# Kernel optimization log

Measured on AMD Instinct MI355X. Metric: run time of the kernel, lower is better.

## Reference

```python
import jax, jax.numpy as jnp
import numpy as np

N, E, H, C = 50000, 800000, 4, 64   # nodes, edges, heads, per-head channels
EMB, VOCAB, G, RD, OUT = 128, 512, 64, 64, 1
LEAKY_SLOPE = 0.2


def _gat_layer(h_in, src, dst, W, att_src, att_dst, bias):
    """PyG GATConv, concat=False (mean over heads), eval mode (no dropout)."""
    n = h_in.shape[0]
    h = (h_in @ W).reshape(n, H, C)                       # [N,H,C]
    a_src = jnp.sum(h * att_src, axis=-1)                 # [N,H]
    a_dst = jnp.sum(h * att_dst, axis=-1)                 # [N,H]
    e = jax.nn.leaky_relu(a_src[src] + a_dst[dst], LEAKY_SLOPE)  # [E',H]
    # segment softmax over incoming edges of each destination node
    m = jax.ops.segment_max(e, dst, num_segments=n)       # [N,H]
    m = jnp.where(jnp.isfinite(m), m, 0.0)
    p = jnp.exp(e - m[dst])                               # [E',H]
    s = jax.ops.segment_sum(p, dst, num_segments=n)       # [N,H]
    alpha = p / (s[dst] + 1e-16)                          # [E',H]
    msg = alpha[:, :, None] * h[src]                      # [E',H,C]
    out = jax.ops.segment_sum(msg, dst, num_segments=n)   # [N,H,C]
    return out.mean(axis=1) + bias                        # [N,C]


def setup_inputs() -> dict:
    key = jax.random.key(0)
    ks = jax.random.split(key, 16)
    x = jax.random.randint(ks[0], (N, 2), 0, VOCAB)
    edge_index = jax.random.randint(ks[1], (2, E), 0, N)
    batch = jnp.sort(jax.random.randint(ks[2], (N,), 0, G))
    f32 = jnp.float32
    emb = jax.random.normal(ks[3], (VOCAB, EMB), f32) * (EMB ** -0.5)
    W0 = jax.random.normal(ks[4], (EMB, H * C), f32) * (EMB ** -0.5)
    as0 = jax.random.normal(ks[5], (H, C), f32) * (C ** -0.5)
    ad0 = jax.random.normal(ks[6], (H, C), f32) * (C ** -0.5)
    b0 = jnp.zeros((C,), f32)
    W1 = jax.random.normal(ks[7], (C, H * C), f32) * (C ** -0.5)
    as1 = jax.random.normal(ks[8], (H, C), f32) * (C ** -0.5)
    ad1 = jax.random.normal(ks[9], (H, C), f32) * (C ** -0.5)
    b1 = jnp.zeros((C,), f32)
    W2 = jax.random.normal(ks[10], (C, H * C), f32) * (C ** -0.5)
    as2 = jax.random.normal(ks[11], (H, C), f32) * (C ** -0.5)
    ad2 = jax.random.normal(ks[12], (H, C), f32) * (C ** -0.5)
    b2 = jnp.zeros((C,), f32)
    mW1 = jax.random.normal(ks[13], (C, C), f32) * (C ** -0.5)
    mb1 = jnp.zeros((C,), f32)
    mW2 = jax.random.normal(ks[14], (C, RD), f32) * (C ** -0.5)
    mb2 = jnp.zeros((RD,), f32)
    rW = jax.random.normal(ks[15], (RD, OUT), f32) * (RD ** -0.5)
    rb = jnp.zeros((OUT,), f32)
    return dict(x=x, edge_index=edge_index, batch=batch, emb=emb,
                W0=W0, as0=as0, ad0=ad0, b0=b0,
                W1=W1, as1=as1, ad1=ad1, b1=b1,
                W2=W2, as2=as2, ad2=ad2, b2=b2,
                mW1=mW1, mb1=mb1, mW2=mW2, mb2=mb2, rW=rW, rb=rb)


def reference(x, edge_index, batch, emb,
              W0, as0, ad0, b0,
              W1, as1, ad1, b1,
              W2, as2, ad2, b2,
              mW1, mb1, mW2, mb2, rW, rb):
    n = x.shape[0]
    # add self-loops (PyG GATConv default)
    loops = jnp.arange(n)
    src = jnp.concatenate([edge_index[0], loops])
    dst = jnp.concatenate([edge_index[1], loops])

    h = emb[x[:, 0]]                                      # [N,EMB]
    h = jax.nn.elu(_gat_layer(h, src, dst, W0, as0, ad0, b0))
    h = jax.nn.elu(_gat_layer(h, src, dst, W1, as1, ad1, b1))
    h = jax.nn.elu(_gat_layer(h, src, dst, W2, as2, ad2, b2))

    # global mean pool per graph
    sums = jax.ops.segment_sum(h, batch, num_segments=G)  # [G,C]
    cnt = jax.ops.segment_sum(jnp.ones((n,), h.dtype), batch, num_segments=G)
    pooled = sums / jnp.maximum(cnt, 1.0)[:, None]

    # MLP readout: Linear -> ELU -> Linear (plain last, eval: no dropout)
    r = jax.nn.elu(pooled @ mW1 + mb1)
    r = r @ mW2 + mb2
    return r @ rW + rb                                     # [G,OUT]
```

## Files before the change

kernel.cpp:

```cpp
#include <hip/hip_runtime.h>
#include <hip/hip_bf16.h>

#define TPB 256
#define CHUNK 8


__global__ void gather_emb_k(const int* __restrict__ x, const float* __restrict__ emb,
                             float* __restrict__ h0, int n) {
  int idx = blockIdx.x * TPB + threadIdx.x;
  if (idx >= n * 128) return;
  int node = idx >> 7, k = idx & 127;
  h0[idx] = emb[x[node * 2] * 128 + k];
}

__global__ void edge_hist_k(const int* __restrict__ ei, int* __restrict__ deg, int E, int n) {
  int e = blockIdx.x * TPB + threadIdx.x;
  if (e >= E + n) return;
  int dst = (e < E) ? ei[E + e] : (e - E);
  atomicAdd(&deg[dst], 1);
}

__global__ void scan_block_k(const int* __restrict__ deg, int* __restrict__ row_ptr,
                             int* __restrict__ bsum, int n) {
  __shared__ int buf[TPB];
  int t = threadIdx.x, base = blockIdx.x * TPB;
  int v = (base + t < n) ? deg[base + t] : 0;
  buf[t] = v;
  __syncthreads();
  for (int off = 1; off < TPB; off <<= 1) {
    int xv = (t >= off) ? buf[t - off] : 0;
    __syncthreads();
    buf[t] += xv;
    __syncthreads();
  }
  if (base + t < n) row_ptr[base + t + 1] = buf[t];
  if (t == TPB - 1) bsum[blockIdx.x] = buf[t];
}

__global__ void scan_bsum_k(int* __restrict__ bsum, int B) {
  __shared__ int buf[TPB];
  int t = threadIdx.x;
  int v = (t < B) ? bsum[t] : 0;
  buf[t] = v;
  __syncthreads();
  for (int off = 1; off < TPB; off <<= 1) {
    int xv = (t >= off) ? buf[t - off] : 0;
    __syncthreads();
    buf[t] += xv;
    __syncthreads();
  }
  if (t < B) bsum[t] = buf[t] - v;
}

__global__ void scan_add_k(int* __restrict__ row_ptr, const int* __restrict__ bsum, int n) {
  int idx = blockIdx.x * TPB + threadIdx.x;
  if (idx == 0) row_ptr[0] = 0;
  if (idx < n) row_ptr[idx + 1] += bsum[idx >> 8];
}

__global__ void edge_scatter_k(const int* __restrict__ ei, const int* __restrict__ row_ptr,
                               int* __restrict__ cursor, int* __restrict__ csr_src,
                               int E, int n) {
  int e = blockIdx.x * TPB + threadIdx.x;
  if (e >= E + n) return;
  int src, dst;
  if (e < E) { src = ei[e]; dst = ei[E + e]; }
  else       { src = e - E; dst = e - E; }
  int pos = atomicAdd(&cursor[dst], 1);
  csr_src[row_ptr[dst] + pos] = src;
}

template <int K>
__global__ __launch_bounds__(TPB) void gemm_hw_k(const float* __restrict__ h,
                                                 const float* __restrict__ W,
                                                 float* __restrict__ hW, int n) {
  int t = threadIdx.x;
  int n0 = blockIdx.x * 16;
  float acc[16];
#pragma unroll
  for (int i = 0; i < 16; i++) acc[i] = 0.f;
  const float* hb = h + (size_t)n0 * K;
  for (int k0 = 0; k0 < K; k0 += 8) {
    float wv[8];
#pragma unroll
    for (int kk = 0; kk < 8; kk++) wv[kk] = W[(k0 + kk) * 256 + t];
#pragma unroll
    for (int i = 0; i < 16; i++) {
#pragma unroll
      for (int kk = 0; kk < 8; kk++)
        acc[i] = fmaf(hb[i * K + k0 + kk], wv[kk], acc[i]);
    }
  }
  float* outp = hW + (size_t)n0 * 256 + t;
#pragma unroll
  for (int i = 0; i < 16; i++)
    if (n0 + i < n) outp[i * 256] = acc[i];
}

__global__ void attn_coef_k(const float* __restrict__ hW, const float* __restrict__ as,
                            const float* __restrict__ ad, float* __restrict__ a_srcv,
                            float* __restrict__ a_dstv, int n) {
  int idx = blockIdx.x * TPB + threadIdx.x;
  if (idx >= n * 4) return;
  int node = idx >> 2, hh = idx & 3;
  const float* row = hW + (size_t)node * 256 + hh * 64;
  const float* asr = as + hh * 64;
  const float* adr = ad + hh * 64;
  float s = 0.f, d = 0.f;
#pragma unroll 8
  for (int c = 0; c < 64; c++) {
    float v = row[c];
    s = fmaf(v, asr[c], s);
    d = fmaf(v, adr[c], d);
  }
  a_srcv[idx] = s;
  a_dstv[idx] = d;
}

__global__ __launch_bounds__(TPB) void gat_agg_k(
    const float* __restrict__ hW, const float* __restrict__ a_srcv,
    const float* __restrict__ a_dstv, const int* __restrict__ row_ptr,
    const int* __restrict__ csr_src, const float* __restrict__ bias,
    float* __restrict__ h_out, int n) {
  int node = blockIdx.x;
  int t = threadIdx.x;
  int w = t >> 6;
  int l = t & 63;
  int hh = l >> 4;
  int beg = row_ptr[node], end = row_ptr[node + 1];
  float ad = a_dstv[node * 4 + hh];

  float m = -1e30f, ssum = 0.f;
  float ax = 0.f, ay = 0.f, az = 0.f, aw = 0.f;

  for (int base = beg + w; base < end; base += 4 * CHUNK) {
    int   ss[CHUNK];
    float ee[CHUNK];
    float4 hv[CHUNK];
#pragma unroll
    for (int j = 0; j < CHUNK; j++) {
      int k = base + j * 4;
      ss[j] = (k < end) ? csr_src[k] : -1;
    }
#pragma unroll
    for (int j = 0; j < CHUNK; j++) {
      if (ss[j] >= 0) {
        float e = a_srcv[ss[j] * 4 + hh] + ad;
        ee[j] = (e >= 0.f) ? e : 0.2f * e;
        hv[j] = *reinterpret_cast<const float4*>(hW + (size_t)ss[j] * 256 + l * 4);
      } else {
        ee[j] = -1e30f;
        hv[j] = make_float4(0.f, 0.f, 0.f, 0.f);
      }
    }
#pragma unroll
    for (int j = 0; j < CHUNK; j++) {
      float e = ee[j];
      float diff = e - m;
      float ex = __expf(-fabsf(diff));
      bool nm = diff > 0.f;
      float scale = nm ? ex : 1.f;
      float p     = nm ? 1.f : ex;
      m = nm ? e : m;
      ssum = fmaf(ssum, scale, p);
      ax = fmaf(ax, scale, p * hv[j].x);
      ay = fmaf(ay, scale, p * hv[j].y);
      az = fmaf(az, scale, p * hv[j].z);
      aw = fmaf(aw, scale, p * hv[j].w);
    }
  }

  __shared__ float m_sh[4][4];
  __shared__ float s_sh[4][4];
  __shared__ float red[4][256];
  if ((l & 15) == 0) m_sh[w][hh] = m;
  __syncthreads();
  float mt = fmaxf(fmaxf(m_sh[0][hh], m_sh[1][hh]), fmaxf(m_sh[2][hh], m_sh[3][hh]));
  float sc = __expf(m - mt);
  if ((l & 15) == 0) s_sh[w][hh] = ssum * sc;
  float* rw = &red[w][l * 4];
  rw[0] = ax * sc; rw[1] = ay * sc; rw[2] = az * sc; rw[3] = aw * sc;
  __syncthreads();

  if (t < 64) {
    float o = 0.f;
#pragma unroll
    for (int h = 0; h < 4; ++h) {
      int cc = h * 64 + t;
      float v = red[0][cc] + red[1][cc] + red[2][cc] + red[3][cc];
      float st = s_sh[0][h] + s_sh[1][h] + s_sh[2][h] + s_sh[3][h];
      o += v / (st + 1e-16f);
    }
    o = o * 0.25f + bias[t];
    o = (o > 0.f) ? o : (expf(o) - 1.f);
    h_out[node * 64 + t] = o;
  }
}

__global__ void group_bounds_k(const int* __restrict__ batch, int* __restrict__ gstart,
                               int G_, int n) {
  int i = blockIdx.x * TPB + threadIdx.x;
  if (i >= n) return;
  if (i == 0) {
    int b0 = batch[0];
    for (int g = 0; g <= b0; ++g) gstart[g] = 0;
  } else {
    int bp = batch[i - 1], bc = batch[i];
    for (int g = bp + 1; g <= bc; ++g) gstart[g] = i;
  }
  if (i == n - 1) {
    int bl = batch[n - 1];
    for (int g = bl + 1; g <= G_; ++g) gstart[g] = n;
  }
}

__global__ void pool_group_k(const float* __restrict__ h, const int* __restrict__ gstart,
                             float* __restrict__ pooled) {
  int g = blockIdx.x, t = threadIdx.x;
  int c = t & 63, sub = t >> 6;
  int beg = gstart[g], end = gstart[g + 1];
  float s = 0.f;
  for (int i = beg + sub; i < end; i += 4) s += h[(size_t)i * 64 + c];
  __shared__ float red[4][64];
  red[sub][c] = s;
  __syncthreads();
  if (t < 64) {
    float v = red[0][t] + red[1][t] + red[2][t] + red[3][t];
    float cn = fmaxf((float)(end - beg), 1.f);
    pooled[g * 64 + t] = v / cn;
  }
}

__global__ void readout_k(const float* __restrict__ pooled,
                          const float* __restrict__ mW1, const float* __restrict__ mb1,
                          const float* __restrict__ mW2, const float* __restrict__ mb2,
                          const float* __restrict__ rW, const float* __restrict__ rb,
                          float* __restrict__ out) {
  int g = blockIdx.x, t = threadIdx.x;
  __shared__ float pm[64], r1[64], r2[64];
  pm[t] = pooled[g * 64 + t];
  __syncthreads();
  float a = mb1[t];
  for (int c = 0; c < 64; c++) a = fmaf(pm[c], mW1[c * 64 + t], a);
  a = (a > 0.f) ? a : (expf(a) - 1.f);
  r1[t] = a;
  __syncthreads();
  float b = mb2[t];
  for (int c = 0; c < 64; c++) b = fmaf(r1[c], mW2[c * 64 + t], b);
  r2[t] = b;
  __syncthreads();
  if (t == 0) {
    float o = rb[0];
    for (int c = 0; c < 64; c++) o = fmaf(r2[c], rW[c], o);
    out[g] = o;
  }
}

extern "C" void kernel_launch(void* const* d_in, const int* in_sizes, int n_in,
                              void* d_out, int out_size, void* d_ws, size_t ws_size,
                              hipStream_t stream) {
  const int* x     = (const int*)d_in[0];
  const int* ei    = (const int*)d_in[1];
  const int* batch = (const int*)d_in[2];
  const float* emb = (const float*)d_in[3];
  const float* W0  = (const float*)d_in[4];
  const float* as0 = (const float*)d_in[5];
  const float* ad0 = (const float*)d_in[6];
  const float* b0  = (const float*)d_in[7];
  const float* W1  = (const float*)d_in[8];
  const float* as1 = (const float*)d_in[9];
  const float* ad1 = (const float*)d_in[10];
  const float* b1  = (const float*)d_in[11];
  const float* W2  = (const float*)d_in[12];
  const float* as2 = (const float*)d_in[13];
  const float* ad2 = (const float*)d_in[14];
  const float* b2  = (const float*)d_in[15];
  const float* mW1 = (const float*)d_in[16];
  const float* mb1 = (const float*)d_in[17];
  const float* mW2 = (const float*)d_in[18];
  const float* mb2 = (const float*)d_in[19];
  const float* rW  = (const float*)d_in[20];
  const float* rb  = (const float*)d_in[21];
  float* out = (float*)d_out;

  const int N = in_sizes[2];
  const int E = in_sizes[1] / 2;
  const int TOT = E + N;
  const int G = out_size;

  char* p = (char*)d_ws;
  auto alloc = [&](size_t bytes) {
    void* r = (void*)p;
    p += (bytes + 255) & ~(size_t)255;
    return r;
  };
  float* hA      = (float*)alloc((size_t)(N + 16) * 128 * 4);
  float* hWbuf   = (float*)alloc((size_t)(N + 16) * 256 * 4);
  float* hB      = (float*)alloc((size_t)(N + 16) * 64 * 4);
  float* a_srcv  = (float*)alloc((size_t)N * 4 * 4);
  float* a_dstv  = (float*)alloc((size_t)N * 4 * 4);
  int*   deg     = (int*)alloc((size_t)N * 4);
  int*   row_ptr = (int*)alloc((size_t)(N + 1) * 4);
  int*   bsum    = (int*)alloc(256 * 4);
  int*   csr     = (int*)alloc((size_t)TOT * 4);
  float* pooled  = (float*)alloc((size_t)G * 64 * 4);
  int*   gstart  = (int*)alloc((size_t)(G + 1) * 4);

  int gTOT = (TOT + TPB - 1) / TPB;
  int gN   = (N + TPB - 1) / TPB;
  int B    = gN;

  hipMemsetAsync(deg, 0, (size_t)N * 4, stream);
  edge_hist_k<<<gTOT, TPB, 0, stream>>>(ei, deg, E, N);
  scan_block_k<<<B, TPB, 0, stream>>>(deg, row_ptr, bsum, N);
  scan_bsum_k<<<1, TPB, 0, stream>>>(bsum, B);
  scan_add_k<<<gN, TPB, 0, stream>>>(row_ptr, bsum, N);
  hipMemsetAsync(deg, 0, (size_t)N * 4, stream);
  edge_scatter_k<<<gTOT, TPB, 0, stream>>>(ei, row_ptr, deg, csr, E, N);

  group_bounds_k<<<gN, TPB, 0, stream>>>(batch, gstart, G, N);

  gather_emb_k<<<(N * 128 + TPB - 1) / TPB, TPB, 0, stream>>>(x, emb, hA, N);

  int gGemm = (N + 15) / 16;
  int gCoef = (N * 4 + TPB - 1) / TPB;

  gemm_hw_k<128><<<gGemm, TPB, 0, stream>>>(hA, W0, hWbuf, N);
  attn_coef_k<<<gCoef, TPB, 0, stream>>>(hWbuf, as0, ad0, a_srcv, a_dstv, N);
  gat_agg_k<<<N, TPB, 0, stream>>>(hWbuf, a_srcv, a_dstv, row_ptr, csr, b0, hB, N);
  gemm_hw_k<64><<<gGemm, TPB, 0, stream>>>(hB, W1, hWbuf, N);
  attn_coef_k<<<gCoef, TPB, 0, stream>>>(hWbuf, as1, ad1, a_srcv, a_dstv, N);
  gat_agg_k<<<N, TPB, 0, stream>>>(hWbuf, a_srcv, a_dstv, row_ptr, csr, b1, hA, N);
  gemm_hw_k<64><<<gGemm, TPB, 0, stream>>>(hA, W2, hWbuf, N);
  attn_coef_k<<<gCoef, TPB, 0, stream>>>(hWbuf, as2, ad2, a_srcv, a_dstv, N);
  gat_agg_k<<<N, TPB, 0, stream>>>(hWbuf, a_srcv, a_dstv, row_ptr, csr, b2, hB, N);

  pool_group_k<<<G, TPB, 0, stream>>>(hB, gstart, pooled);
  readout_k<<<G, 64, 0, stream>>>(pooled, mW1, mb1, mW2, mb2, rW, rb, out);
}
```

Measured before the change: 897.1 us.

## Map one wavefront per destination node in GAT aggregation, drop LDS reduction

The aggregation kernel now gives each 64-lane wavefront its own destination node (four nodes per block) instead of splitting one node's edges across four wavefronts. This removes the shared-memory cross-wave reduction and both block barriers, and the head mean becomes a shuffle-xor reduction followed by a float4 store. Attention logits are prescaled by log2(e) so the online softmax can use the hardware exp2 with a simpler max-based update. The trade-off is less parallelism per node, since each wave walks all of a node's edges serially, which could hurt on high-degree nodes.

```diff
diff --git a/kernel.cpp b/kernel.cpp
--- a/kernel.cpp
+++ b/kernel.cpp
@@ -3,6 +3,11 @@
 
 #define TPB 256
 #define CHUNK 8
+#define LOG2E 1.4426950408889634f
+
+__device__ __forceinline__ float fast_exp2(float x) {
+  return __builtin_amdgcn_exp2f(x);
+}
 
 
 __global__ void gather_emb_k(const int* __restrict__ x, const float* __restrict__ emb,
@@ -113,8 +118,8 @@
     s = fmaf(v, asr[c], s);
     d = fmaf(v, adr[c], d);
   }
-  a_srcv[idx] = s;
-  a_dstv[idx] = d;
+  a_srcv[idx] = s * LOG2E;
+  a_dstv[idx] = d * LOG2E;
 }
 
 __global__ __launch_bounds__(TPB) void gat_agg_k(
@@ -122,10 +127,10 @@
     const float* __restrict__ a_dstv, const int* __restrict__ row_ptr,
     const int* __restrict__ csr_src, const float* __restrict__ bias,
     float* __restrict__ h_out, int n) {
-  int node = blockIdx.x;
-  int t = threadIdx.x;
-  int w = t >> 6;
-  int l = t & 63;
+  int w = threadIdx.x >> 6;
+  int node = blockIdx.x * 4 + w;
+  if (node >= n) return;
+  int l = threadIdx.x & 63;
   int hh = l >> 4;
   int beg = row_ptr[node], end = row_ptr[node + 1];
   float ad = a_dstv[node * 4 + hh];
@@ -133,13 +138,13 @@
   float m = -1e30f, ssum = 0.f;
   float ax = 0.f, ay = 0.f, az = 0.f, aw = 0.f;
 
-  for (int base = beg + w; base < end; base += 4 * CHUNK) {
+  for (int base = beg; base < end; base += CHUNK) {
     int   ss[CHUNK];
     float ee[CHUNK];
     float4 hv[CHUNK];
 #pragma unroll
     for (int j = 0; j < CHUNK; j++) {
-      int k = base + j * 4;
+      int k = base + j;
       ss[j] = (k < end) ? csr_src[k] : -1;
     }
 #pragma unroll
@@ -155,45 +160,42 @@
     }
 #pragma unroll
     for (int j = 0; j < CHUNK; j++) {
-      float e = ee[j];
-      float diff = e - m;
-      float ex = __expf(-fabsf(diff));
-      bool nm = diff > 0.f;
-      float scale = nm ? ex : 1.f;
-      float p     = nm ? 1.f : ex;
-      m = nm ? e : m;
-      ssum = fmaf(ssum, scale, p);
-      ax = fmaf(ax, scale, p * hv[j].x);
-      ay = fmaf(ay, scale, p * hv[j].y);
-      az = fmaf(az, scale, p * hv[j].z);
-      aw = fmaf(aw, scale, p * hv[j].w);
+      float e  = ee[j];
+      float mn = fmaxf(m, e);
+      float sc = fast_exp2(m - mn);
+      float p  = fast_exp2(e - mn);
+      m = mn;
+      ssum = fmaf(ssum, sc, p);
+      ax = fmaf(ax, sc, p * hv[j].x);
+      ay = fmaf(ay, sc, p * hv[j].y);
+      az = fmaf(az, sc, p * hv[j].z);
+      aw = fmaf(aw, sc, p * hv[j].w);
     }
   }
 
-  __shared__ float m_sh[4][4];
-  __shared__ float s_sh[4][4];
-  __shared__ float red[4][256];
-  if ((l & 15) == 0) m_sh[w][hh] = m;
-  __syncthreads();
-  float mt = fmaxf(fmaxf(m_sh[0][hh], m_sh[1][hh]), fmaxf(m_sh[2][hh], m_sh[3][hh]));
-  float sc = __expf(m - mt);
-  if ((l & 15) == 0) s_sh[w][hh] = ssum * sc;
-  float* rw = &red[w][l * 4];
-  rw[0] = ax * sc; rw[1] = ay * sc; rw[2] = az * sc; rw[3] = aw * sc;
-  __syncthreads();
-
-  if (t < 64) {
-    float o = 0.f;
-#pragma unroll
-    for (int h = 0; h < 4; ++h) {
-      int cc = h * 64 + t;
-      float v = red[0][cc] + red[1][cc] + red[2][cc] + red[3][cc];
-      float st = s_sh[0][h] + s_sh[1][h] + s_sh[2][h] + s_sh[3][h];
-      o += v / (st + 1e-16f);
-    }
-    o = o * 0.25f + bias[t];
-    o = (o > 0.f) ? o : (expf(o) - 1.f);
-    h_out[node * 64 + t] = o;
+  float inv = 1.f / (ssum + 1e-16f);
+  float o0 = ax * inv, o1 = ay * inv, o2 = az * inv, o3 = aw * inv;
+
+#pragma unroll
+  for (int mask = 16; mask <= 32; mask <<= 1) {
+    o0 += __shfl_xor(o0, mask, 64);
+    o1 += __shfl_xor(o1, mask, 64);
+    o2 += __shfl_xor(o2, mask, 64);
+    o3 += __shfl_xor(o3, mask, 64);
+  }
+
+  if (l < 16) {
+    const float4 bv = *reinterpret_cast<const float4*>(bias + l * 4);
+    float4 o;
+    o.x = o0 * 0.25f + bv.x;
+    o.y = o1 * 0.25f + bv.y;
+    o.z = o2 * 0.25f + bv.z;
+    o.w = o3 * 0.25f + bv.w;
+    o.x = (o.x > 0.f) ? o.x : (expf(o.x) - 1.f);
+    o.y = (o.y > 0.f) ? o.y : (expf(o.y) - 1.f);
+    o.z = (o.z > 0.f) ? o.z : (expf(o.z) - 1.f);
+    o.w = (o.w > 0.f) ? o.w : (expf(o.w) - 1.f);
+    *reinterpret_cast<float4*>(h_out + (size_t)node * 64 + l * 4) = o;
   }
 }
 
@@ -310,12 +312,12 @@
   int gN   = (N + TPB - 1) / TPB;
   int B    = gN;
 
-  hipMemsetAsync(deg, 0, (size_t)N * 4, stream);
+  (void)hipMemsetAsync(deg, 0, (size_t)N * 4, stream);
   edge_hist_k<<<gTOT, TPB, 0, stream>>>(ei, deg, E, N);
   scan_block_k<<<B, TPB, 0, stream>>>(deg, row_ptr, bsum, N);
   scan_bsum_k<<<1, TPB, 0, stream>>>(bsum, B);
   scan_add_k<<<gN, TPB, 0, stream>>>(row_ptr, bsum, N);
-  hipMemsetAsync(deg, 0, (size_t)N * 4, stream);
+  (void)hipMemsetAsync(deg, 0, (size_t)N * 4, stream);
   edge_scatter_k<<<gTOT, TPB, 0, stream>>>(ei, row_ptr, deg, csr, E, N);
 
   group_bounds_k<<<gN, TPB, 0, stream>>>(batch, gstart, G, N);
@@ -324,16 +326,17 @@
 
   int gGemm = (N + 15) / 16;
   int gCoef = (N * 4 + TPB - 1) / TPB;
+  int gAgg  = (N + 3) / 4;
 
   gemm_hw_k<128><<<gGemm, TPB, 0, stream>>>(hA, W0, hWbuf, N);
   attn_coef_k<<<gCoef, TPB, 0, stream>>>(hWbuf, as0, ad0, a_srcv, a_dstv, N);
-  gat_agg_k<<<N, TPB, 0, stream>>>(hWbuf, a_srcv, a_dstv, row_ptr, csr, b0, hB, N);
+  gat_agg_k<<<gAgg, TPB, 0, stream>>>(hWbuf, a_srcv, a_dstv, row_ptr, csr, b0, hB, N);
   gemm_hw_k<64><<<gGemm, TPB, 0, stream>>>(hB, W1, hWbuf, N);
   attn_coef_k<<<gCoef, TPB, 0, stream>>>(hWbuf, as1, ad1, a_srcv, a_dstv, N);
-  gat_agg_k<<<N, TPB, 0, stream>>>(hWbuf, a_srcv, a_dstv, row_ptr, csr, b1, hA, N);
+  gat_agg_k<<<gAgg, TPB, 0, stream>>>(hWbuf, a_srcv, a_dstv, row_ptr, csr, b1, hA, N);
   gemm_hw_k<64><<<gGemm, TPB, 0, stream>>>(hA, W2, hWbuf, N);
   attn_coef_k<<<gCoef, TPB, 0, stream>>>(hWbuf, as2, ad2, a_srcv, a_dstv, N);
-  gat_agg_k<<<N, TPB, 0, stream>>>(hWbuf, a_srcv, a_dstv, row_ptr, csr, b2, hB, N);
+  gat_agg_k<<<gAgg, TPB, 0, stream>>>(hWbuf, a_srcv, a_dstv, row_ptr, csr, b2, hB, N);
 
   pool_group_k<<<G, TPB, 0, stream>>>(hB, gstart, pooled);
   readout_k<<<G, 64, 0, stream>>>(pooled, mW1, mb1, mW2, mb2, rW, rb, out);
```

Result: no change. 902.4 us (+0.6%).
